# Kernel optimization log

Measured on AMD Instinct MI355X. Metric: run time of the kernel, lower is better.

## Reference

```python
import jax, jax.numpy as jnp
import numpy as np

N = 100000
E = 1600000
F_IN = 128
HID = 32
HEADS = 4
NCLS = 64
NEG_SLOPE = 0.2
EPS = 1e-16


def setup_inputs() -> dict:
    key = jax.random.key(0)
    ks = jax.random.split(key, 12)
    inp = jax.random.normal(ks[0], (N, F_IN), dtype=jnp.float32)
    edge_index = jax.random.randint(ks[1], (2, E), 0, N, dtype=jnp.int64)
    s1 = 1.0 / np.sqrt(F_IN)
    W1 = jax.random.uniform(ks[2], (F_IN, HEADS, HID), jnp.float32, -s1, s1)
    att_src1 = jax.random.normal(ks[3], (HEADS, HID), dtype=jnp.float32) * s1
    att_dst1 = jax.random.normal(ks[4], (HEADS, HID), dtype=jnp.float32) * s1
    bias1 = jnp.zeros((HEADS * HID,), dtype=jnp.float32)
    d2 = HEADS * HID
    s2 = 1.0 / np.sqrt(d2)
    W2 = jax.random.uniform(ks[5], (d2, 1, NCLS), jnp.float32, -s2, s2)
    att_src2 = jax.random.normal(ks[6], (1, NCLS), dtype=jnp.float32) * s2
    att_dst2 = jax.random.normal(ks[7], (1, NCLS), dtype=jnp.float32) * s2
    bias2 = jnp.zeros((NCLS,), dtype=jnp.float32)
    return {"inp": inp, "edge_index": edge_index, "W1": W1, "att_src1": att_src1,
            "att_dst1": att_dst1, "bias1": bias1, "W2": W2, "att_src2": att_src2,
            "att_dst2": att_dst2, "bias2": bias2}


def _gat_layer(x, src, dst, W, a_src, a_dst, bias):
    # x: [N, F]; W: [F, H, C]
    h = jnp.einsum('nf,fhc->nhc', x, W)            # [N, H, C]
    a_s = jnp.sum(h * a_src[None], axis=-1)        # [N, H]
    a_d = jnp.sum(h * a_dst[None], axis=-1)        # [N, H]
    e = a_s[src] + a_d[dst]                        # [Etot, H]
    e = jnp.where(e >= 0, e, NEG_SLOPE * e)        # LeakyReLU(0.2)
    # softmax normalized per destination node (segment softmax)
    m = jax.ops.segment_max(e, dst, num_segments=N)      # [N, H]
    ex = jnp.exp(e - m[dst])
    denom = jax.ops.segment_sum(ex, dst, num_segments=N)  # [N, H]
    alpha = ex / (denom[dst] + EPS)                # [Etot, H]
    msg = h[src] * alpha[..., None]                # [Etot, H, C]
    out = jax.ops.segment_sum(msg, dst, num_segments=N)   # [N, H, C]
    return out.reshape(N, -1) + bias


def reference(inp, edge_index, W1, att_src1, att_dst1, bias1, W2, att_src2, att_dst2, bias2):
    # add self-loops (PyG GATConv default)
    loop = jnp.arange(N, dtype=edge_index.dtype)
    src = jnp.concatenate([edge_index[0], loop])
    dst = jnp.concatenate([edge_index[1], loop])
    x = _gat_layer(inp, src, dst, W1, att_src1, att_dst1, bias1)   # [N, H*HID]
    x = _gat_layer(x, src, dst, W2, att_src2, att_dst2, bias2)     # [N, NCLS]
    return x
```

## Files before the change

kernel.cpp:

```cpp
#include <hip/hip_runtime.h>

#define N_NODES 100000
#define F1 128
#define NCLS 64
#define EPB 8

typedef __attribute__((ext_vector_type(8))) short bf16x8;
typedef __attribute__((ext_vector_type(4))) float f32x4;

__device__ __forceinline__ unsigned f2bf(float x) {
    unsigned u = __builtin_bit_cast(unsigned, x);
    u += 0x7fff + ((u >> 16) & 1);
    return u >> 16;
}
__device__ __forceinline__ float bflo(unsigned u) {
    return __builtin_bit_cast(float, u << 16);
}
__device__ __forceinline__ float bfhi(unsigned u) {
    return __builtin_bit_cast(float, u & 0xffff0000u);
}

#define SWZ_I(v, off) __builtin_amdgcn_ds_swizzle((v), (off))
#define SWZ_F(v, off) __builtin_bit_cast(float, __builtin_amdgcn_ds_swizzle(__builtin_bit_cast(int, (v)), (off)))

__global__ void detect_kernel(const int* __restrict__ ei, int* __restrict__ flag) {
    int tid = threadIdx.x;
    int v = ei[2 * tid + 1];
    unsigned long long ball = __ballot(v == 0);
    if (tid == 0) *flag = (ball == ~0ull) ? 1 : 0;
}

__device__ __forceinline__ int load_edge(const int* ei, int is64, long long idx) {
    return is64 ? ei[2 * idx] : ei[idx];
}

__global__ __launch_bounds__(256) void histA_kernel(
        const int* __restrict__ ei, const int* __restrict__ flag,
        int* __restrict__ ghBM, int EB, int E) {
    __shared__ int bins[256];
    int tid = threadIdx.x;
    bins[tid] = 0;
    __syncthreads();
    long long base = (long long)blockIdx.x * 2048 + tid * EPB;
    int is64 = *flag;
    int d[EPB];
    #pragma unroll
    for (int k = 0; k < EPB; ++k) {
        long long e = base + k;
        d[k] = (e < E) ? load_edge(ei, is64, (long long)E + e) : -1;
    }
    #pragma unroll
    for (int k = 0; k < EPB; ++k)
        if (d[k] >= 0) atomicAdd(&bins[d[k] >> 9], 1);
    __syncthreads();
    ghBM[(size_t)tid * EB + blockIdx.x] = bins[tid];
}

#define SCAN_BLOCK 1024
__global__ void pscanA_kernel(int* __restrict__ g, int* __restrict__ bsum, int K) {
    __shared__ int sm[SCAN_BLOCK];
    int tid = threadIdx.x;
    int i = blockIdx.x * SCAN_BLOCK + tid;
    int v = (i < K) ? g[i] : 0;
    sm[tid] = v;
    __syncthreads();
    for (int off = 1; off < SCAN_BLOCK; off <<= 1) {
        int t = (tid >= off) ? sm[tid - off] : 0;
        __syncthreads();
        sm[tid] += t;
        __syncthreads();
    }
    if (i < K) g[i] = sm[tid] - v;
    if (tid == SCAN_BLOCK - 1) bsum[blockIdx.x] = sm[tid];
}

__global__ void pscanB_kernel(int* __restrict__ bsum, int nb) {
    __shared__ int sm[256];
    int tid = threadIdx.x;
    int v = (tid < nb) ? bsum[tid] : 0;
    sm[tid] = v;
    __syncthreads();
    for (int off = 1; off < 256; off <<= 1) {
        int t = (tid >= off) ? sm[tid - off] : 0;
        __syncthreads();
        sm[tid] += t;
        __syncthreads();
    }
    if (tid < nb) bsum[tid] = sm[tid] - v;
}

__global__ void pscanC_kernel(int* __restrict__ g, const int* __restrict__ bsum, int K) {
    int i = blockIdx.x * SCAN_BLOCK + threadIdx.x;
    if (i < K) g[i] += bsum[blockIdx.x];
}

__global__ __launch_bounds__(256) void scatterB_kernel(
        const int* __restrict__ ei, const int* __restrict__ flag,
        const int* __restrict__ ghBM, int EB,
        unsigned* __restrict__ tmp, int E) {
    __shared__ int base[256];
    int tid = threadIdx.x;
    base[tid] = ghBM[(size_t)tid * EB + blockIdx.x];
    __syncthreads();
    long long eb = (long long)blockIdx.x * 2048 + tid * EPB;
    int is64 = *flag;
    int d[EPB], s[EPB];
    #pragma unroll
    for (int k = 0; k < EPB; ++k) {
        long long e = eb + k;
        d[k] = (e < E) ? load_edge(ei, is64, (long long)E + e) : -1;
    }
    #pragma unroll
    for (int k = 0; k < EPB; ++k) {
        long long e = eb + k;
        s[k] = (e < E) ? load_edge(ei, is64, e) : 0;
    }
    #pragma unroll
    for (int k = 0; k < EPB; ++k) {
        if (d[k] >= 0) {
            int pos = atomicAdd(&base[d[k] >> 9], 1);
            tmp[pos] = (unsigned)s[k] | ((unsigned)(d[k] & 511) << 17);
        }
    }
}

__global__ __launch_bounds__(256) void bucketC_kernel(
        const unsigned* __restrict__ tmp, const int* __restrict__ ghBM, int EB,
        int* __restrict__ row_ptr, int* __restrict__ col, int E, int n) {
    __shared__ int lb[512];
    __shared__ int lo[512];
    __shared__ int sm[256];
    int bk = blockIdx.x;
    int tid = threadIdx.x;
    int gbase = ghBM[(size_t)bk * EB];
    int gend = (bk == 255) ? E : ghBM[(size_t)(bk + 1) * EB];
    int cnt = gend - gbase;
    lb[tid] = 0; lb[tid + 256] = 0;
    __syncthreads();
    for (int i = tid; i < cnt; i += 256)
        atomicAdd(&lb[tmp[gbase + i] >> 17], 1);
    __syncthreads();
    int p = lb[2 * tid], q = lb[2 * tid + 1];
    int ps = p + q;
    sm[tid] = ps;
    __syncthreads();
    for (int off = 1; off < 256; off <<= 1) {
        int t = (tid >= off) ? sm[tid - off] : 0;
        __syncthreads();
        sm[tid] += t;
        __syncthreads();
    }
    int excl = sm[tid] - ps;
    int e0 = excl, e1 = excl + p;
    lo[2 * tid] = e0; lo[2 * tid + 1] = e1;
    int v0 = bk * 512 + 2 * tid;
    if (v0 <= n) row_ptr[v0] = gbase + e0;
    if (v0 + 1 <= n) row_ptr[v0 + 1] = gbase + e1;
    __syncthreads();
    for (int i = tid; i < cnt; i += 256) {
        unsigned v = tmp[gbase + i];
        int r = atomicAdd(&lo[v >> 17], 1);
        col[gbase + r] = (int)(v & 0x1FFFFu);
    }
}

__global__ __launch_bounds__(256) void gemm1_kernel(
        const float* __restrict__ x, const float* __restrict__ W,
        const float* __restrict__ att_s, const float* __restrict__ att_d,
        unsigned* __restrict__ hp, float* __restrict__ as_, float* __restrict__ ad_, int n) {
    __shared__ uint4 WtS[2048];
    unsigned* Wt = (unsigned*)WtS;
    int tid = threadIdx.x;
    {
        int ch = tid & 127, fb = tid >> 7;
        #pragma unroll
        for (int j8 = 0; j8 < 8; ++j8) {
            int f0 = fb * 64 + j8 * 8;
            unsigned pk[4];
            #pragma unroll
            for (int p = 0; p < 4; ++p) {
                float lo = W[(size_t)(f0 + 2 * p) * 128 + ch];
                float hi = W[(size_t)(f0 + 2 * p + 1) * 128 + ch];
                pk[p] = f2bf(lo) | (f2bf(hi) << 16);
            }
            int bcol = (f0 * 2) ^ ((ch & 7) << 4);
            *(uint4*)&Wt[ch * 64 + (bcol >> 2)] = *(uint4*)pk;
        }
    }
    __syncthreads();
    int lane = tid & 63, w = tid >> 6;
    int col = lane & 15, quad = lane >> 4;
    int nodebase = blockIdx.x * 128 + w * 32;
    bf16x8 a[2][4];
    #pragma unroll
    for (int s = 0; s < 2; ++s) {
        int node = nodebase + s * 16 + col;
        const float* xr = x + (size_t)node * 128;
        bool v = node < n;
        #pragma unroll
        for (int kk = 0; kk < 4; ++kk) {
            float4 lo = v ? *(const float4*)&xr[kk * 32 + quad * 8]
                          : make_float4(0.f, 0.f, 0.f, 0.f);
            float4 hi = v ? *(const float4*)&xr[kk * 32 + quad * 8 + 4]
                          : make_float4(0.f, 0.f, 0.f, 0.f);
            unsigned pk[4];
            pk[0] = f2bf(lo.x) | (f2bf(lo.y) << 16);
            pk[1] = f2bf(lo.z) | (f2bf(lo.w) << 16);
            pk[2] = f2bf(hi.x) | (f2bf(hi.y) << 16);
            pk[3] = f2bf(hi.z) | (f2bf(hi.w) << 16);
            a[s][kk] = *(bf16x8*)pk;
        }
    }
    f32x4 acc[2][8] = {};
    #pragma unroll
    for (int c = 0; c < 8; ++c) {
        int brow = c * 16 + col;
        bf16x8 b[4];
        #pragma unroll
        for (int kk = 0; kk < 4; ++kk) {
            int bcol = (kk * 64 + quad * 16) ^ ((brow & 7) << 4);
            b[kk] = *(bf16x8*)&Wt[brow * 64 + (bcol >> 2)];
        }
        #pragma unroll
        for (int s = 0; s < 2; ++s)
            #pragma unroll
            for (int kk = 0; kk < 4; ++kk)
                acc[s][c] = __builtin_amdgcn_mfma_f32_16x16x32_bf16(a[s][kk], b[kk], acc[s][c], 0, 0, 0);
    }
    float aS[8], aD[8];
    #pragma unroll
    for (int c = 0; c < 8; ++c) { aS[c] = att_s[c * 16 + col]; aD[c] = att_d[c * 16 + col]; }
    #pragma unroll
    for (int s = 0; s < 2; ++s) {
        #pragma unroll
        for (int c = 0; c < 8; ++c) {
            #pragma unroll
            for (int r = 0; r < 4; ++r) {
                float own = acc[s][c][r];
                float par = SWZ_F(own, 0x041F);
                int node = nodebase + s * 16 + quad * 4 + r;
                if (!(lane & 1) && node < n)
                    hp[(size_t)node * 64 + c * 8 + (col >> 1)] =
                        f2bf(own) | (f2bf(par) << 16);
            }
        }
        #pragma unroll
        for (int h = 0; h < 4; ++h) {
            #pragma unroll
            for (int r = 0; r < 4; ++r) {
                float ps = acc[s][2 * h][r] * aS[2 * h] + acc[s][2 * h + 1][r] * aS[2 * h + 1];
                float pd = acc[s][2 * h][r] * aD[2 * h] + acc[s][2 * h + 1][r] * aD[2 * h + 1];
                ps += SWZ_F(ps, 0x041F); pd += SWZ_F(pd, 0x041F);
                ps += SWZ_F(ps, 0x081F); pd += SWZ_F(pd, 0x081F);
                ps += SWZ_F(ps, 0x101F); pd += SWZ_F(pd, 0x101F);
                ps += SWZ_F(ps, 0x201F); pd += SWZ_F(pd, 0x201F);
                int node = nodebase + s * 16 + quad * 4 + r;
                if (col == 0 && node < n) {
                    as_[(size_t)node * 4 + h] = ps;
                    ad_[(size_t)node * 4 + h] = pd;
                }
            }
        }
    }
}

__global__ __launch_bounds__(256) void gemm2_kernel(
        const unsigned* __restrict__ xp, const float* __restrict__ W,
        const float* __restrict__ att_s, const float* __restrict__ att_d,
        unsigned* __restrict__ hp, float* __restrict__ as_, float* __restrict__ ad_, int n) {
    __shared__ uint4 WtS[1024];
    unsigned* Wt = (unsigned*)WtS;
    int tid = threadIdx.x;
    {
        int ch = tid & 63, fb = tid >> 6;
        #pragma unroll
        for (int j8 = 0; j8 < 4; ++j8) {
            int f0 = fb * 32 + j8 * 8;
            unsigned pk[4];
            #pragma unroll
            for (int p = 0; p < 4; ++p) {
                float lo = W[(size_t)(f0 + 2 * p) * 64 + ch];
                float hi = W[(size_t)(f0 + 2 * p + 1) * 64 + ch];
                pk[p] = f2bf(lo) | (f2bf(hi) << 16);
            }
            int bcol = (f0 * 2) ^ ((ch & 7) << 4);
            *(uint4*)&Wt[ch * 64 + (bcol >> 2)] = *(uint4*)pk;
        }
    }
    __syncthreads();
    int lane = tid & 63, w = tid >> 6;
    int col = lane & 15, quad = lane >> 4;
    int nodebase = blockIdx.x * 128 + w * 32;
    bf16x8 a[2][4];
    #pragma unroll
    for (int s = 0; s < 2; ++s) {
        int node = nodebase + s * 16 + col;
        bool v = node < n;
        #pragma unroll
        for (int kk = 0; kk < 4; ++kk) {
            uint4 u = v ? *(const uint4*)&xp[(size_t)node * 64 + kk * 16 + quad * 4]
                        : make_uint4(0, 0, 0, 0);
            a[s][kk] = *(bf16x8*)&u;
        }
    }
    f32x4 acc[2][4] = {};
    #pragma unroll
    for (int c = 0; c < 4; ++c) {
        int brow = c * 16 + col;
        bf16x8 b[4];
        #pragma unroll
        for (int kk = 0; kk < 4; ++kk) {
            int bcol = (kk * 64 + quad * 16) ^ ((brow & 7) << 4);
            b[kk] = *(bf16x8*)&Wt[brow * 64 + (bcol >> 2)];
        }
        #pragma unroll
        for (int s = 0; s < 2; ++s)
            #pragma unroll
            for (int kk = 0; kk < 4; ++kk)
                acc[s][c] = __builtin_amdgcn_mfma_f32_16x16x32_bf16(a[s][kk], b[kk], acc[s][c], 0, 0, 0);
    }
    float aS[4], aD[4];
    #pragma unroll
    for (int c = 0; c < 4; ++c) { aS[c] = att_s[c * 16 + col]; aD[c] = att_d[c * 16 + col]; }
    #pragma unroll
    for (int s = 0; s < 2; ++s) {
        #pragma unroll
        for (int c = 0; c < 4; ++c) {
            #pragma unroll
            for (int r = 0; r < 4; ++r) {
                float own = acc[s][c][r];
                float par = SWZ_F(own, 0x041F);
                int node = nodebase + s * 16 + quad * 4 + r;
                if (!(lane & 1) && node < n)
                    hp[(size_t)node * 32 + c * 8 + (col >> 1)] =
                        f2bf(own) | (f2bf(par) << 16);
            }
        }
        #pragma unroll
        for (int r = 0; r < 4; ++r) {
            float ps = 0.f, pd = 0.f;
            #pragma unroll
            for (int c = 0; c < 4; ++c) {
                ps = fmaf(acc[s][c][r], aS[c], ps);
                pd = fmaf(acc[s][c][r], aD[c], pd);
            }
            ps += SWZ_F(ps, 0x041F); pd += SWZ_F(pd, 0x041F);
            ps += SWZ_F(ps, 0x081F); pd += SWZ_F(pd, 0x081F);
            ps += SWZ_F(ps, 0x101F); pd += SWZ_F(pd, 0x101F);
            ps += SWZ_F(ps, 0x201F); pd += SWZ_F(pd, 0x201F);
            int node = nodebase + s * 16 + quad * 4 + r;
            if (col == 0 && node < n) { as_[node] = ps; ad_[node] = pd; }
        }
    }
}

#define A1_G8(B, K0) { \
    int t0 = SWZ_I(myc, (((B)+(K0)+0)<<5)); \
    int t1 = SWZ_I(myc, (((B)+(K0)+1)<<5)); \
    int t2 = SWZ_I(myc, (((B)+(K0)+2)<<5)); \
    int t3 = SWZ_I(myc, (((B)+(K0)+3)<<5)); \
    int t4 = SWZ_I(myc, (((B)+(K0)+4)<<5)); \
    int t5 = SWZ_I(myc, (((B)+(K0)+5)<<5)); \
    int t6 = SWZ_I(myc, (((B)+(K0)+6)<<5)); \
    int t7 = SWZ_I(myc, (((B)+(K0)+7)<<5)); \
    unsigned v0 = hp[(size_t)t0 * 64 + lane]; \
    unsigned v1 = hp[(size_t)t1 * 64 + lane]; \
    unsigned v2 = hp[(size_t)t2 * 64 + lane]; \
    unsigned v3 = hp[(size_t)t3 * 64 + lane]; \
    unsigned v4 = hp[(size_t)t4 * 64 + lane]; \
    unsigned v5 = hp[(size_t)t5 * 64 + lane]; \
    unsigned v6 = hp[(size_t)t6 * 64 + lane]; \
    unsigned v7 = hp[(size_t)t7 * 64 + lane]; \
    float q0 = SWZ_F(ew, ((((K0)+0)<<5)|0x10)); \
    float q1 = SWZ_F(ew, ((((K0)+1)<<5)|0x10)); \
    float q2 = SWZ_F(ew, ((((K0)+2)<<5)|0x10)); \
    float q3 = SWZ_F(ew, ((((K0)+3)<<5)|0x10)); \
    float q4 = SWZ_F(ew, ((((K0)+4)<<5)|0x10)); \
    float q5 = SWZ_F(ew, ((((K0)+5)<<5)|0x10)); \
    float q6 = SWZ_F(ew, ((((K0)+6)<<5)|0x10)); \
    float q7 = SWZ_F(ew, ((((K0)+7)<<5)|0x10)); \
    s += q0; acc0 = fmaf(q0, bflo(v0), acc0); acc1 = fmaf(q0, bfhi(v0), acc1); \
    s += q1; acc0 = fmaf(q1, bflo(v1), acc0); acc1 = fmaf(q1, bfhi(v1), acc1); \
    s += q2; acc0 = fmaf(q2, bflo(v2), acc0); acc1 = fmaf(q2, bfhi(v2), acc1); \
    s += q3; acc0 = fmaf(q3, bflo(v3), acc0); acc1 = fmaf(q3, bfhi(v3), acc1); \
    s += q4; acc0 = fmaf(q4, bflo(v4), acc0); acc1 = fmaf(q4, bfhi(v4), acc1); \
    s += q5; acc0 = fmaf(q5, bflo(v5), acc0); acc1 = fmaf(q5, bfhi(v5), acc1); \
    s += q6; acc0 = fmaf(q6, bflo(v6), acc0); acc1 = fmaf(q6, bfhi(v6), acc1); \
    s += q7; acc0 = fmaf(q7, bflo(v7), acc0); acc1 = fmaf(q7, bfhi(v7), acc1); }

#define A1_SUB(B) { \
    int sspec = SWZ_I(myc, (((B)<<5) | 0x0F)); \
    float ee_ = as_[(size_t)sspec * 4 + head] + adv; \
    ee_ = fmaxf(ee_, 0.2f * ee_); \
    float ew = ((cb + (B) + (lane & 15)) < end) ? __expf(ee_) : 0.f; \
    A1_G8(B, 0) \
    if (m > (B) + 8) A1_G8(B, 8) }

__global__ __launch_bounds__(256) void agg1_kernel(
        const unsigned* __restrict__ hp, const float* __restrict__ as_,
        const float* __restrict__ ad_, const int* __restrict__ row_ptr,
        const int* __restrict__ col, const float* __restrict__ bias,
        unsigned* __restrict__ outp, int n) {
    int wid = (blockIdx.x * 256 + threadIdx.x) >> 6;
    int lane = threadIdx.x & 63;
    if (wid >= n) return;
    int node = wid;
    int head = lane >> 4;
    float adv = ad_[(size_t)node * 4 + head];
    float e0 = as_[(size_t)node * 4 + head] + adv;
    e0 = fmaxf(e0, 0.2f * e0);
    float w0 = __expf(e0);
    float s = w0;
    unsigned u0 = hp[(size_t)node * 64 + lane];
    float acc0 = w0 * bflo(u0), acc1 = w0 * bfhi(u0);
    int beg = row_ptr[node], end = row_ptr[node + 1];
    for (int cb = beg; cb < end; cb += 32) {
        int m = end - cb; if (m > 32) m = 32;
        int ci = cb + (lane & 31);
        int myc = col[(ci < end) ? ci : (end - 1)];
        A1_SUB(0)
        if (m > 16) A1_SUB(16)
    }
    float inv = 1.0f / (s + 1e-16f);
    float2 b = *(const float2*)&bias[lane * 2];
    outp[(size_t)node * 64 + lane] =
        f2bf(acc0 * inv + b.x) | (f2bf(acc1 * inv + b.y) << 16);
}

#define A2_G4(K0) { \
    int t0 = SWZ_I(myc, (((K0)+0)<<5)); \
    int t1 = SWZ_I(myc, (((K0)+1)<<5)); \
    int t2 = SWZ_I(myc, (((K0)+2)<<5)); \
    int t3 = SWZ_I(myc, (((K0)+3)<<5)); \
    unsigned v0 = hp[(size_t)t0 * 32 + wrd]; \
    unsigned v1 = hp[(size_t)t1 * 32 + wrd]; \
    unsigned v2 = hp[(size_t)t2 * 32 + wrd]; \
    unsigned v3 = hp[(size_t)t3 * 32 + wrd]; \
    float q0 = SWZ_F(ew, (((K0)+0)<<5)); \
    float q1 = SWZ_F(ew, (((K0)+1)<<5)); \
    float q2 = SWZ_F(ew, (((K0)+2)<<5)); \
    float q3 = SWZ_F(ew, (((K0)+3)<<5)); \
    s += q0; acc0 = fmaf(q0, bflo(v0), acc0); acc1 = fmaf(q0, bfhi(v0), acc1); \
    s += q1; acc0 = fmaf(q1, bflo(v1), acc0); acc1 = fmaf(q1, bfhi(v1), acc1); \
    s += q2; acc0 = fmaf(q2, bflo(v2), acc0); acc1 = fmaf(q2, bfhi(v2), acc1); \
    s += q3; acc0 = fmaf(q3, bflo(v3), acc0); acc1 = fmaf(q3, bfhi(v3), acc1); }

__global__ __launch_bounds__(256) void agg2_kernel(
        const unsigned* __restrict__ hp, const float* __restrict__ as_,
        const float* __restrict__ ad_, const int* __restrict__ row_ptr,
        const int* __restrict__ col, const float* __restrict__ bias,
        float* __restrict__ out, int n) {
    int wid = (blockIdx.x * 256 + threadIdx.x) >> 6;
    int lane = threadIdx.x & 63;
    if (wid >= n) return;
    int node = wid;
    int half = lane >> 5, wrd = lane & 31;
    float adv = ad_[node];
    float s = 0.f, acc0 = 0.f, acc1 = 0.f;
    {
        float e = as_[node] + adv; e = fmaxf(e, 0.2f * e);
        float w = __expf(e);
        if (half == 0) {
            unsigned u = hp[(size_t)node * 32 + wrd];
            s = w; acc0 = w * bflo(u); acc1 = w * bfhi(u);
        }
    }
    int beg = row_ptr[node], end = row_ptr[node + 1];
    for (int cb = beg; cb < end; cb += 64) {
        int m = end - cb; if (m > 64) m = 64;
        int idx = cb + 2 * (lane & 31) + half;
        int myc = col[(idx < end) ? idx : (end - 1)];
        float ee = as_[myc] + adv; ee = fmaxf(ee, 0.2f * ee);
        float ew = (idx < end) ? __expf(ee) : 0.f;
        A2_G4(0)
        if (m > 8)  A2_G4(4)
        if (m > 16) A2_G4(8)
        if (m > 24) A2_G4(12)
        if (m > 32) {
            A2_G4(16)
            if (m > 40) A2_G4(20)
            if (m > 48) A2_G4(24)
            if (m > 56) A2_G4(28)
        }
    }
    s += __shfl_xor(s, 32);
    acc0 += __shfl_xor(acc0, 32);
    acc1 += __shfl_xor(acc1, 32);
    if (half == 0) {
        float inv = 1.0f / (s + 1e-16f);
        float2 b = *(const float2*)&bias[wrd * 2];
        *(float2*)&out[(size_t)node * 64 + wrd * 2] =
            make_float2(acc0 * inv + b.x, acc1 * inv + b.y);
    }
}

extern "C" void kernel_launch(void* const* d_in, const int* in_sizes, int n_in,
                              void* d_out, int out_size, void* d_ws, size_t ws_size,
                              hipStream_t stream) {
    const float* inp   = (const float*)d_in[0];
    const int*   ei    = (const int*)d_in[1];
    const float* W1    = (const float*)d_in[2];
    const float* atts1 = (const float*)d_in[3];
    const float* attd1 = (const float*)d_in[4];
    const float* bias1 = (const float*)d_in[5];
    const float* W2    = (const float*)d_in[6];
    const float* atts2 = (const float*)d_in[7];
    const float* attd2 = (const float*)d_in[8];
    const float* bias2 = (const float*)d_in[9];
    float* out = (float*)d_out;

    const int N = N_NODES;
    const int E = in_sizes[1] / 2;

    const int EB = (E + 2047) / 2048;
    const int K = 256 * EB;
    const int nbK = (K + SCAN_BLOCK - 1) / SCAN_BLOCK;

    unsigned* h1p = (unsigned*)d_ws;
    unsigned* x1p = h1p + (size_t)N * 64;
    float* as1 = (float*)(x1p + (size_t)N * 64);
    float* ad1 = as1 + (size_t)N * 4;
    int* row_ptr  = (int*)(ad1 + (size_t)N * 4);
    int* col      = row_ptr + N + 1;
    int* ghBM     = col + E;
    int* bsum     = ghBM + K;
    int* flag     = bsum + 256;
    unsigned* tmp = x1p;

    detect_kernel<<<1, 64, 0, stream>>>(ei, flag);

    histA_kernel<<<EB, 256, 0, stream>>>(ei, flag, ghBM, EB, E);
    pscanA_kernel<<<nbK, SCAN_BLOCK, 0, stream>>>(ghBM, bsum, K);
    pscanB_kernel<<<1, 256, 0, stream>>>(bsum, nbK);
    pscanC_kernel<<<nbK, SCAN_BLOCK, 0, stream>>>(ghBM, bsum, K);
    scatterB_kernel<<<EB, 256, 0, stream>>>(ei, flag, ghBM, EB, tmp, E);
    bucketC_kernel<<<256, 256, 0, stream>>>(tmp, ghBM, EB, row_ptr, col, E, N);

    gemm1_kernel<<<(N + 127) / 128, 256, 0, stream>>>(inp, W1, atts1, attd1, h1p, as1, ad1, N);
    agg1_kernel<<<(N + 3) / 4, 256, 0, stream>>>(h1p, as1, ad1, row_ptr, col, bias1, x1p, N);

    gemm2_kernel<<<(N + 127) / 128, 256, 0, stream>>>(x1p, W2, atts2, attd2, h1p, as1, ad1, N);
    agg2_kernel<<<(N + 3) / 4, 256, 0, stream>>>(h1p, as1, ad1, row_ptr, col, bias2, out, N);
}
```

Baseline: 220.8 us.

## Fuse edge scatter with gemm1, merge scan phases, inline dtype probe

Removes the separate edge-dtype detect kernel by probing in each block via ballot. Folds the block-sum scan into the add-back kernel: each block re-scans the small bsum array itself. Combines the edge scatter and the first GEMM into a single heterogeneous grid, so these independent stages overlap and fewer kernels are launched. In exchange, each block repeats some redundant probe and scan work, and the larger fused kernel may have higher register and LDS use.

```diff
diff --git a/kernel.cpp b/kernel.cpp
--- a/kernel.cpp
+++ b/kernel.cpp
@@ -23,26 +23,25 @@
 #define SWZ_I(v, off) __builtin_amdgcn_ds_swizzle((v), (off))
 #define SWZ_F(v, off) __builtin_bit_cast(float, __builtin_amdgcn_ds_swizzle(__builtin_bit_cast(int, (v)), (off)))
 
-__global__ void detect_kernel(const int* __restrict__ ei, int* __restrict__ flag) {
-    int tid = threadIdx.x;
-    int v = ei[2 * tid + 1];
-    unsigned long long ball = __ballot(v == 0);
-    if (tid == 0) *flag = (ball == ~0ull) ? 1 : 0;
-}
-
 __device__ __forceinline__ int load_edge(const int* ei, int is64, long long idx) {
     return is64 ? ei[2 * idx] : ei[idx];
 }
 
+#define EDGE_PROBE(ei, s_is64, tid) { \
+    int v_ = (ei)[2 * ((tid) & 63) + 1]; \
+    unsigned long long b_ = __ballot(v_ == 0); \
+    if ((tid) == 0) s_is64 = (b_ == ~0ull) ? 1 : 0; }
+
 __global__ __launch_bounds__(256) void histA_kernel(
-        const int* __restrict__ ei, const int* __restrict__ flag,
-        int* __restrict__ ghBM, int EB, int E) {
+        const int* __restrict__ ei, int* __restrict__ ghBM, int EB, int E) {
     __shared__ int bins[256];
+    __shared__ int s_is64;
     int tid = threadIdx.x;
     bins[tid] = 0;
-    __syncthreads();
+    EDGE_PROBE(ei, s_is64, tid)
+    __syncthreads();
+    int is64 = s_is64;
     long long base = (long long)blockIdx.x * 2048 + tid * EPB;
-    int is64 = *flag;
     int d[EPB];
     #pragma unroll
     for (int k = 0; k < EPB; ++k) {
@@ -74,52 +73,149 @@
     if (tid == SCAN_BLOCK - 1) bsum[blockIdx.x] = sm[tid];
 }
 
-__global__ void pscanB_kernel(int* __restrict__ bsum, int nb) {
+__global__ void pscanC_kernel(int* __restrict__ g, const int* __restrict__ bsum,
+                              int K, int nb) {
     __shared__ int sm[256];
     int tid = threadIdx.x;
-    int v = (tid < nb) ? bsum[tid] : 0;
-    sm[tid] = v;
+    if (tid < 256) sm[tid] = (tid < nb) ? bsum[tid] : 0;
     __syncthreads();
     for (int off = 1; off < 256; off <<= 1) {
-        int t = (tid >= off) ? sm[tid - off] : 0;
-        __syncthreads();
-        sm[tid] += t;
-        __syncthreads();
-    }
-    if (tid < nb) bsum[tid] = sm[tid] - v;
-}
-
-__global__ void pscanC_kernel(int* __restrict__ g, const int* __restrict__ bsum, int K) {
-    int i = blockIdx.x * SCAN_BLOCK + threadIdx.x;
-    if (i < K) g[i] += bsum[blockIdx.x];
-}
-
-__global__ __launch_bounds__(256) void scatterB_kernel(
-        const int* __restrict__ ei, const int* __restrict__ flag,
-        const int* __restrict__ ghBM, int EB,
-        unsigned* __restrict__ tmp, int E) {
-    __shared__ int base[256];
+        int t = (tid < 256 && tid >= off) ? sm[tid - off] : 0;
+        __syncthreads();
+        if (tid < 256) sm[tid] += t;
+        __syncthreads();
+    }
+    int pre = (blockIdx.x == 0) ? 0 : sm[blockIdx.x - 1];
+    int i = blockIdx.x * SCAN_BLOCK + tid;
+    if (i < K) g[i] += pre;
+}
+
+__global__ __launch_bounds__(256) void scatgemm1_kernel(
+        const int* __restrict__ ei, const int* __restrict__ ghBM, int EB,
+        unsigned* __restrict__ tmp, int E,
+        const float* __restrict__ x, const float* __restrict__ W,
+        const float* __restrict__ att_s, const float* __restrict__ att_d,
+        unsigned* __restrict__ hp, float* __restrict__ as_, float* __restrict__ ad_, int n) {
+    __shared__ uint4 WtS[2048];
+    __shared__ int s_is64;
     int tid = threadIdx.x;
-    base[tid] = ghBM[(size_t)tid * EB + blockIdx.x];
-    __syncthreads();
-    long long eb = (long long)blockIdx.x * 2048 + tid * EPB;
-    int is64 = *flag;
-    int d[EPB], s[EPB];
-    #pragma unroll
-    for (int k = 0; k < EPB; ++k) {
-        long long e = eb + k;
-        d[k] = (e < E) ? load_edge(ei, is64, (long long)E + e) : -1;
-    }
-    #pragma unroll
-    for (int k = 0; k < EPB; ++k) {
-        long long e = eb + k;
-        s[k] = (e < E) ? load_edge(ei, is64, e) : 0;
-    }
-    #pragma unroll
-    for (int k = 0; k < EPB; ++k) {
-        if (d[k] >= 0) {
-            int pos = atomicAdd(&base[d[k] >> 9], 1);
-            tmp[pos] = (unsigned)s[k] | ((unsigned)(d[k] & 511) << 17);
+    if (blockIdx.x < (unsigned)EB) {
+        int* base = (int*)WtS;
+        base[tid] = ghBM[(size_t)tid * EB + blockIdx.x];
+        EDGE_PROBE(ei, s_is64, tid)
+        __syncthreads();
+        int is64 = s_is64;
+        long long eb = (long long)blockIdx.x * 2048 + tid * EPB;
+        int d[EPB], s[EPB];
+        #pragma unroll
+        for (int k = 0; k < EPB; ++k) {
+            long long e = eb + k;
+            d[k] = (e < E) ? load_edge(ei, is64, (long long)E + e) : -1;
+        }
+        #pragma unroll
+        for (int k = 0; k < EPB; ++k) {
+            long long e = eb + k;
+            s[k] = (e < E) ? load_edge(ei, is64, e) : 0;
+        }
+        #pragma unroll
+        for (int k = 0; k < EPB; ++k) {
+            if (d[k] >= 0) {
+                int pos = atomicAdd(&base[d[k] >> 9], 1);
+                tmp[pos] = (unsigned)s[k] | ((unsigned)(d[k] & 511) << 17);
+            }
+        }
+        return;
+    }
+    unsigned* Wt = (unsigned*)WtS;
+    {
+        int ch = tid & 127, fb = tid >> 7;
+        #pragma unroll
+        for (int j8 = 0; j8 < 8; ++j8) {
+            int f0 = fb * 64 + j8 * 8;
+            unsigned pk[4];
+            #pragma unroll
+            for (int p = 0; p < 4; ++p) {
+                float lo = W[(size_t)(f0 + 2 * p) * 128 + ch];
+                float hi = W[(size_t)(f0 + 2 * p + 1) * 128 + ch];
+                pk[p] = f2bf(lo) | (f2bf(hi) << 16);
+            }
+            int bcol = (f0 * 2) ^ ((ch & 7) << 4);
+            *(uint4*)&Wt[ch * 64 + (bcol >> 2)] = *(uint4*)pk;
+        }
+    }
+    __syncthreads();
+    int lane = tid & 63, w = tid >> 6;
+    int col = lane & 15, quad = lane >> 4;
+    int nodebase = (blockIdx.x - EB) * 128 + w * 32;
+    bf16x8 a[2][4];
+    #pragma unroll
+    for (int s = 0; s < 2; ++s) {
+        int node = nodebase + s * 16 + col;
+        const float* xr = x + (size_t)node * 128;
+        bool v = node < n;
+        #pragma unroll
+        for (int kk = 0; kk < 4; ++kk) {
+            float4 lo = v ? *(const float4*)&xr[kk * 32 + quad * 8]
+                          : make_float4(0.f, 0.f, 0.f, 0.f);
+            float4 hi = v ? *(const float4*)&xr[kk * 32 + quad * 8 + 4]
+                          : make_float4(0.f, 0.f, 0.f, 0.f);
+            unsigned pk[4];
+            pk[0] = f2bf(lo.x) | (f2bf(lo.y) << 16);
+            pk[1] = f2bf(lo.z) | (f2bf(lo.w) << 16);
+            pk[2] = f2bf(hi.x) | (f2bf(hi.y) << 16);
+            pk[3] = f2bf(hi.z) | (f2bf(hi.w) << 16);
+            a[s][kk] = *(bf16x8*)pk;
+        }
+    }
+    f32x4 acc[2][8] = {};
+    #pragma unroll
+    for (int c = 0; c < 8; ++c) {
+        int brow = c * 16 + col;
+        bf16x8 b[4];
+        #pragma unroll
+        for (int kk = 0; kk < 4; ++kk) {
+            int bcol = (kk * 64 + quad * 16) ^ ((brow & 7) << 4);
+            b[kk] = *(bf16x8*)&Wt[brow * 64 + (bcol >> 2)];
+        }
+        #pragma unroll
+        for (int s = 0; s < 2; ++s)
+            #pragma unroll
+            for (int kk = 0; kk < 4; ++kk)
+                acc[s][c] = __builtin_amdgcn_mfma_f32_16x16x32_bf16(a[s][kk], b[kk], acc[s][c], 0, 0, 0);
+    }
+    float aS[8], aD[8];
+    #pragma unroll
+    for (int c = 0; c < 8; ++c) { aS[c] = att_s[c * 16 + col]; aD[c] = att_d[c * 16 + col]; }
+    #pragma unroll
+    for (int s = 0; s < 2; ++s) {
+        #pragma unroll
+        for (int c = 0; c < 8; ++c) {
+            #pragma unroll
+            for (int r = 0; r < 4; ++r) {
+                float own = acc[s][c][r];
+                float par = SWZ_F(own, 0x041F);
+                int node = nodebase + s * 16 + quad * 4 + r;
+                if (!(lane & 1) && node < n)
+                    hp[(size_t)node * 64 + c * 8 + (col >> 1)] =
+                        f2bf(own) | (f2bf(par) << 16);
+            }
+        }
+        #pragma unroll
+        for (int h = 0; h < 4; ++h) {
+            #pragma unroll
+            for (int r = 0; r < 4; ++r) {
+                float ps = acc[s][2 * h][r] * aS[2 * h] + acc[s][2 * h + 1][r] * aS[2 * h + 1];
+                float pd = acc[s][2 * h][r] * aD[2 * h] + acc[s][2 * h + 1][r] * aD[2 * h + 1];
+                ps += SWZ_F(ps, 0x041F); pd += SWZ_F(pd, 0x041F);
+                ps += SWZ_F(ps, 0x081F); pd += SWZ_F(pd, 0x081F);
+                ps += SWZ_F(ps, 0x101F); pd += SWZ_F(pd, 0x101F);
+                ps += SWZ_F(ps, 0x201F); pd += SWZ_F(pd, 0x201F);
+                int node = nodebase + s * 16 + quad * 4 + r;
+                if (col == 0 && node < n) {
+                    as_[(size_t)node * 4 + h] = ps;
+                    ad_[(size_t)node * 4 + h] = pd;
+                }
+            }
         }
     }
 }
@@ -161,106 +257,6 @@
         unsigned v = tmp[gbase + i];
         int r = atomicAdd(&lo[v >> 17], 1);
         col[gbase + r] = (int)(v & 0x1FFFFu);
-    }
-}
-
-__global__ __launch_bounds__(256) void gemm1_kernel(
-        const float* __restrict__ x, const float* __restrict__ W,
-        const float* __restrict__ att_s, const float* __restrict__ att_d,
-        unsigned* __restrict__ hp, float* __restrict__ as_, float* __restrict__ ad_, int n) {
-    __shared__ uint4 WtS[2048];
-    unsigned* Wt = (unsigned*)WtS;
-    int tid = threadIdx.x;
-    {
-        int ch = tid & 127, fb = tid >> 7;
-        #pragma unroll
-        for (int j8 = 0; j8 < 8; ++j8) {
-            int f0 = fb * 64 + j8 * 8;
-            unsigned pk[4];
-            #pragma unroll
-            for (int p = 0; p < 4; ++p) {
-                float lo = W[(size_t)(f0 + 2 * p) * 128 + ch];
-                float hi = W[(size_t)(f0 + 2 * p + 1) * 128 + ch];
-                pk[p] = f2bf(lo) | (f2bf(hi) << 16);
-            }
-            int bcol = (f0 * 2) ^ ((ch & 7) << 4);
-            *(uint4*)&Wt[ch * 64 + (bcol >> 2)] = *(uint4*)pk;
-        }
-    }
-    __syncthreads();
-    int lane = tid & 63, w = tid >> 6;
-    int col = lane & 15, quad = lane >> 4;
-    int nodebase = blockIdx.x * 128 + w * 32;
-    bf16x8 a[2][4];
-    #pragma unroll
-    for (int s = 0; s < 2; ++s) {
-        int node = nodebase + s * 16 + col;
-        const float* xr = x + (size_t)node * 128;
-        bool v = node < n;
-        #pragma unroll
-        for (int kk = 0; kk < 4; ++kk) {
-            float4 lo = v ? *(const float4*)&xr[kk * 32 + quad * 8]
-                          : make_float4(0.f, 0.f, 0.f, 0.f);
-            float4 hi = v ? *(const float4*)&xr[kk * 32 + quad * 8 + 4]
-                          : make_float4(0.f, 0.f, 0.f, 0.f);
-            unsigned pk[4];
-            pk[0] = f2bf(lo.x) | (f2bf(lo.y) << 16);
-            pk[1] = f2bf(lo.z) | (f2bf(lo.w) << 16);
-            pk[2] = f2bf(hi.x) | (f2bf(hi.y) << 16);
-            pk[3] = f2bf(hi.z) | (f2bf(hi.w) << 16);
-            a[s][kk] = *(bf16x8*)pk;
-        }
-    }
-    f32x4 acc[2][8] = {};
-    #pragma unroll
-    for (int c = 0; c < 8; ++c) {
-        int brow = c * 16 + col;
-        bf16x8 b[4];
-        #pragma unroll
-        for (int kk = 0; kk < 4; ++kk) {
-            int bcol = (kk * 64 + quad * 16) ^ ((brow & 7) << 4);
-            b[kk] = *(bf16x8*)&Wt[brow * 64 + (bcol >> 2)];
-        }
-        #pragma unroll
-        for (int s = 0; s < 2; ++s)
-            #pragma unroll
-            for (int kk = 0; kk < 4; ++kk)
-                acc[s][c] = __builtin_amdgcn_mfma_f32_16x16x32_bf16(a[s][kk], b[kk], acc[s][c], 0, 0, 0);
-    }
-    float aS[8], aD[8];
-    #pragma unroll
-    for (int c = 0; c < 8; ++c) { aS[c] = att_s[c * 16 + col]; aD[c] = att_d[c * 16 + col]; }
-    #pragma unroll
-    for (int s = 0; s < 2; ++s) {
-        #pragma unroll
-        for (int c = 0; c < 8; ++c) {
-            #pragma unroll
-            for (int r = 0; r < 4; ++r) {
-                float own = acc[s][c][r];
-                float par = SWZ_F(own, 0x041F);
-                int node = nodebase + s * 16 + quad * 4 + r;
-                if (!(lane & 1) && node < n)
-                    hp[(size_t)node * 64 + c * 8 + (col >> 1)] =
-                        f2bf(own) | (f2bf(par) << 16);
-            }
-        }
-        #pragma unroll
-        for (int h = 0; h < 4; ++h) {
-            #pragma unroll
-            for (int r = 0; r < 4; ++r) {
-                float ps = acc[s][2 * h][r] * aS[2 * h] + acc[s][2 * h + 1][r] * aS[2 * h + 1];
-                float pd = acc[s][2 * h][r] * aD[2 * h] + acc[s][2 * h + 1][r] * aD[2 * h + 1];
-                ps += SWZ_F(ps, 0x041F); pd += SWZ_F(pd, 0x041F);
-                ps += SWZ_F(ps, 0x081F); pd += SWZ_F(pd, 0x081F);
-                ps += SWZ_F(ps, 0x101F); pd += SWZ_F(pd, 0x101F);
-                ps += SWZ_F(ps, 0x201F); pd += SWZ_F(pd, 0x201F);
-                int node = nodebase + s * 16 + quad * 4 + r;
-                if (col == 0 && node < n) {
-                    as_[(size_t)node * 4 + h] = ps;
-                    ad_[(size_t)node * 4 + h] = pd;
-                }
-            }
-        }
     }
 }
 
@@ -515,6 +511,7 @@
     const int EB = (E + 2047) / 2048;
     const int K = 256 * EB;
     const int nbK = (K + SCAN_BLOCK - 1) / SCAN_BLOCK;
+    const int nG1 = (N + 127) / 128;
 
     unsigned* h1p = (unsigned*)d_ws;
     unsigned* x1p = h1p + (size_t)N * 64;
@@ -524,19 +521,15 @@
     int* col      = row_ptr + N + 1;
     int* ghBM     = col + E;
     int* bsum     = ghBM + K;
-    int* flag     = bsum + 256;
     unsigned* tmp = x1p;
 
-    detect_kernel<<<1, 64, 0, stream>>>(ei, flag);
-
-    histA_kernel<<<EB, 256, 0, stream>>>(ei, flag, ghBM, EB, E);
+    histA_kernel<<<EB, 256, 0, stream>>>(ei, ghBM, EB, E);
     pscanA_kernel<<<nbK, SCAN_BLOCK, 0, stream>>>(ghBM, bsum, K);
-    pscanB_kernel<<<1, 256, 0, stream>>>(bsum, nbK);
-    pscanC_kernel<<<nbK, SCAN_BLOCK, 0, stream>>>(ghBM, bsum, K);
-    scatterB_kernel<<<EB, 256, 0, stream>>>(ei, flag, ghBM, EB, tmp, E);
+    pscanC_kernel<<<nbK, SCAN_BLOCK, 0, stream>>>(ghBM, bsum, K, nbK);
+    scatgemm1_kernel<<<EB + nG1, 256, 0, stream>>>(
+        ei, ghBM, EB, tmp, E, inp, W1, atts1, attd1, h1p, as1, ad1, N);
     bucketC_kernel<<<256, 256, 0, stream>>>(tmp, ghBM, EB, row_ptr, col, E, N);
 
-    gemm1_kernel<<<(N + 127) / 128, 256, 0, stream>>>(inp, W1, atts1, attd1, h1p, as1, ad1, N);
     agg1_kernel<<<(N + 3) / 4, 256, 0, stream>>>(h1p, as1, ad1, row_ptr, col, bias1, x1p, N);
 
     gemm2_kernel<<<(N + 127) / 128, 256, 0, stream>>>(x1p, W2, atts2, attd2, h1p, as1, ad1, N);
```

Measured after the change: 210.2 us. 4.8% less time.
